# Kernel optimization log

Hardware: AMD Instinct MI355X
Metric: run time of the kernel (lower is better)

## Reference

```python
import jax, jax.numpy as jnp
import numpy as np
import math

HEADS = 6
EPS = 1e-6


def _ln(x, a, b):
    # torch custom LayerNorm: unbiased std, divide by (std + eps)
    m = x.mean(axis=-1, keepdims=True)
    s = jnp.std(x, axis=-1, keepdims=True, ddof=1)
    return a * (x - m) / (s + EPS) + b


def _msa(z, wq, bq, wk, bk, wv, bv, wo, bo):
    B, S, D = z.shape
    dk = D // HEADS
    def proj(w, bias):
        return (z @ w.T + bias).reshape(B, S, HEADS, dk).transpose(0, 2, 1, 3)
    q = proj(wq, bq)  # [B,h,S,dk]
    k = proj(wk, bk)
    v = proj(wv, bv)
    scores = jnp.einsum('bhqd,bhkd->bhqk', q, k) / math.sqrt(dk)  # [B,h,S,S]
    p = jax.nn.softmax(scores, axis=-1)
    o = jnp.einsum('bhqk,bhkd->bhqd', p, v)
    o = o.transpose(0, 2, 1, 3).reshape(B, S, D)
    return o @ wo.T + bo


def setup_inputs() -> dict:
    key = jax.random.key(0)
    ks = jax.random.split(key, 6)
    B, S, D = 2, 4096, 384
    sc = 0.02
    return {
        'x': jax.random.normal(ks[0], (B, S, D), dtype=jnp.float32),
        'a0': jnp.ones((D,), jnp.float32), 'b0': jnp.zeros((D,), jnp.float32),
        'ra0': jnp.ones((D,), jnp.float32), 'rb0': jnp.zeros((D,), jnp.float32),
        'ra1': jnp.ones((D,), jnp.float32), 'rb1': jnp.zeros((D,), jnp.float32),
        'wq': jax.random.normal(ks[1], (D, D), jnp.float32) * sc, 'bq': jnp.zeros((D,), jnp.float32),
        'wk': jax.random.normal(ks[2], (D, D), jnp.float32) * sc, 'bk': jnp.zeros((D,), jnp.float32),
        'wv': jax.random.normal(ks[3], (D, D), jnp.float32) * sc, 'bv': jnp.zeros((D,), jnp.float32),
        'wo': jax.random.normal(ks[4], (D, D), jnp.float32) * sc, 'bo': jnp.zeros((D,), jnp.float32),
    }


def reference(x, a0, b0, ra0, rb0, ra1, rb1, wq, bq, wk, bk, wv, bv, wo, bo):
    # Faithful to source: both residual connections invoke MSA (MLP is never
    # called in the original forward), and the input to MSA is LayerNorm'd
    # twice (residual_conn norm, then norm[0]). Dropout = 0 (eval).
    z = _ln(_ln(x, ra0, rb0), a0, b0)
    x = x + _msa(z, wq, bq, wk, bk, wv, bv, wo, bo)
    z = _ln(_ln(x, ra1, rb1), a0, b0)
    x = x + _msa(z, wq, bq, wk, bk, wv, bv, wo, bo)
    return x
```

## Files before the change

kernel.cpp:

```cpp
#include <hip/hip_runtime.h>
#include <hip/hip_bf16.h>
#include <math.h>

typedef __bf16 bf16;
typedef __bf16 bf16x2 __attribute__((ext_vector_type(2)));
typedef __bf16 bf16x4 __attribute__((ext_vector_type(4)));
typedef __bf16 bf16x8 __attribute__((ext_vector_type(8)));
typedef float  f32x2  __attribute__((ext_vector_type(2)));
typedef float  f32x4  __attribute__((ext_vector_type(4)));
typedef float  f32x16 __attribute__((ext_vector_type(16)));
typedef int    i32x2  __attribute__((ext_vector_type(2)));
typedef int    i32x4  __attribute__((ext_vector_type(4)));

#define SEQ 4096
#define DM  384
#define NH  6
#define DK  64
#define NB  2
#define NSPLIT 4
#define WN  (DM * DM)
#define EPSLN 1e-6f

__device__ __forceinline__ float ldT(const void* p, size_t i, int f32) {
    return f32 ? ((const float*)p)[i] : (float)(((const bf16*)p)[i]);
}

__global__ __launch_bounds__(256) void ln2_kernel(
    const void* __restrict__ x, int xf32,
    const float* __restrict__ ra, const float* __restrict__ rb,
    const float* __restrict__ a0, const float* __restrict__ b0, bf16* __restrict__ z)
{
    int row  = blockIdx.x * 4 + (threadIdx.x >> 6);
    int lane = threadIdx.x & 63;
    size_t base = (size_t)row * DM;

    float v[6];
    float s = 0.f;
    #pragma unroll
    for (int i = 0; i < 6; i++) { v[i] = ldT(x, base + lane + i * 64, xf32); s += v[i]; }
    #pragma unroll
    for (int off = 1; off < 64; off <<= 1) s += __shfl_xor(s, off);
    float m = s * (1.f / DM);
    float sq = 0.f;
    #pragma unroll
    for (int i = 0; i < 6; i++) { float d = v[i] - m; sq += d * d; }
    #pragma unroll
    for (int off = 1; off < 64; off <<= 1) sq += __shfl_xor(sq, off);
    float inv = 1.f / (sqrtf(sq * (1.f / (DM - 1))) + EPSLN);

    s = 0.f;
    #pragma unroll
    for (int i = 0; i < 6; i++) {
        int c = lane + i * 64;
        v[i] = ra[c] * (v[i] - m) * inv + rb[c];
        s += v[i];
    }
    #pragma unroll
    for (int off = 1; off < 64; off <<= 1) s += __shfl_xor(s, off);
    m = s * (1.f / DM);
    sq = 0.f;
    #pragma unroll
    for (int i = 0; i < 6; i++) { float d = v[i] - m; sq += d * d; }
    #pragma unroll
    for (int off = 1; off < 64; off <<= 1) sq += __shfl_xor(sq, off);
    inv = 1.f / (sqrtf(sq * (1.f / (DM - 1))) + EPSLN);

    bf16* zr = z + base;
    #pragma unroll
    for (int i = 0; i < 6; i++) {
        int c = lane + i * 64;
        zr[c] = (bf16)(a0[c] * (v[i] - m) * inv + b0[c]);
    }
}

__global__ __launch_bounds__(256) void qkv_kernel(
    const bf16* __restrict__ A,
    const float* __restrict__ wq, const float* __restrict__ wk, const float* __restrict__ wv,
    const float* __restrict__ bq, const float* __restrict__ bk, const float* __restrict__ bv,
    bf16* __restrict__ qkout, bf16* __restrict__ vt)
{
    const int z = blockIdx.z;
    const float* W    = (z == 0) ? wq : (z == 1) ? wk : wv;
    const float* bias = (z == 0) ? bq : (z == 1) ? bk : bv;

    const int t = threadIdx.x;
    const int wave = t >> 6, lane = t & 63;
    const int l15 = lane & 15, quad = lane >> 4;
    const int wr = wave >> 1, wc = wave & 1;
    const int m0 = blockIdx.x * 128;
    const int n0 = blockIdx.y * 64;

    __shared__ __attribute__((aligned(16))) bf16 As[128][72];
    __shared__ __attribute__((aligned(16))) bf16 Bs[64][72];

    const int r0 = t >> 2;
    const int c0 = (t & 3) * 16;

    const bf16*  aptr0 = A + (size_t)(m0 + r0) * DM + c0;
    const bf16*  aptr1 = A + (size_t)(m0 + 64 + r0) * DM + c0;
    const float* bptr  = W + (size_t)(n0 + r0) * DM + c0;

    bf16x8 ra00 = *(const bf16x8*)(aptr0);
    bf16x8 ra01 = *(const bf16x8*)(aptr0 + 8);
    bf16x8 ra10 = *(const bf16x8*)(aptr1);
    bf16x8 ra11 = *(const bf16x8*)(aptr1 + 8);
    f32x4 wv0 = *(const f32x4*)(bptr);
    f32x4 wv1 = *(const f32x4*)(bptr + 4);
    f32x4 wv2 = *(const f32x4*)(bptr + 8);
    f32x4 wv3 = *(const f32x4*)(bptr + 12);

    f32x4 acc[4][2];
    #pragma unroll
    for (int mi = 0; mi < 4; mi++)
        #pragma unroll
        for (int ni = 0; ni < 2; ni++) acc[mi][ni] = (f32x4){0.f, 0.f, 0.f, 0.f};

    for (int kk = 0; kk < DM; kk += 64) {
        __syncthreads();
        *(bf16x8*)&As[r0][c0]          = ra00;
        *(bf16x8*)&As[r0][c0 + 8]      = ra01;
        *(bf16x8*)&As[64 + r0][c0]     = ra10;
        *(bf16x8*)&As[64 + r0][c0 + 8] = ra11;
        {
            bf16x8 b0v, b1v;
            #pragma unroll
            for (int j = 0; j < 4; j++) {
                b0v[j] = (bf16)wv0[j]; b0v[4 + j] = (bf16)wv1[j];
                b1v[j] = (bf16)wv2[j]; b1v[4 + j] = (bf16)wv3[j];
            }
            *(bf16x8*)&Bs[r0][c0]     = b0v;
            *(bf16x8*)&Bs[r0][c0 + 8] = b1v;
        }
        __syncthreads();
        if (kk + 64 < DM) {
            ra00 = *(const bf16x8*)(aptr0 + kk + 64);
            ra01 = *(const bf16x8*)(aptr0 + kk + 64 + 8);
            ra10 = *(const bf16x8*)(aptr1 + kk + 64);
            ra11 = *(const bf16x8*)(aptr1 + kk + 64 + 8);
            wv0 = *(const f32x4*)(bptr + kk + 64);
            wv1 = *(const f32x4*)(bptr + kk + 64 + 4);
            wv2 = *(const f32x4*)(bptr + kk + 64 + 8);
            wv3 = *(const f32x4*)(bptr + kk + 64 + 12);
        }

        #pragma unroll
        for (int kc = 0; kc < 64; kc += 32) {
            bf16x8 af[4], bf[2];
            #pragma unroll
            for (int mi = 0; mi < 4; mi++)
                af[mi] = *(const bf16x8*)&As[wr * 64 + mi * 16 + l15][kc + quad * 8];
            #pragma unroll
            for (int ni = 0; ni < 2; ni++)
                bf[ni] = *(const bf16x8*)&Bs[wc * 32 + ni * 16 + l15][kc + quad * 8];
            #pragma unroll
            for (int mi = 0; mi < 4; mi++)
                #pragma unroll
                for (int ni = 0; ni < 2; ni++)
                    acc[mi][ni] = __builtin_amdgcn_mfma_f32_16x16x32_bf16(af[mi], bf[ni], acc[mi][ni], 0, 0, 0);
        }
    }

    if (z < 2) {
        bf16* out = qkout + (size_t)z * ((size_t)NB * SEQ * DM);
        #pragma unroll
        for (int ni = 0; ni < 2; ni++) {
            int col = n0 + wc * 32 + ni * 16 + l15;
            float bb = bias[col];
            #pragma unroll
            for (int mi = 0; mi < 4; mi++) {
                #pragma unroll
                for (int r = 0; r < 4; r++) {
                    int row = m0 + wr * 64 + mi * 16 + quad * 4 + r;
                    out[(size_t)row * DM + col] = (bf16)(acc[mi][ni][r] + bb);
                }
            }
        }
    } else {
        #pragma unroll
        for (int ni = 0; ni < 2; ni++) {
            int col = n0 + wc * 32 + ni * 16 + l15;
            int h = col >> 6, d = col & 63;
            float bb = bias[col];
            #pragma unroll
            for (int mi = 0; mi < 4; mi++) {
                int row0 = m0 + wr * 64 + mi * 16 + quad * 4;
                int b = row0 >> 12, s0 = row0 & (SEQ - 1);
                bf16x4 ov;
                #pragma unroll
                for (int r = 0; r < 4; r++) ov[r] = (bf16)(acc[mi][ni][r] + bb);
                *(bf16x4*)(vt + (((size_t)b * NH + h) * DK + d) * SEQ + s0) = ov;
            }
        }
    }
}

__device__ __forceinline__ bf16x8 combineA(
    const bf16* __restrict__ o0, const bf16* __restrict__ o1,
    const bf16* __restrict__ o2, const bf16* __restrict__ o3,
    const float* __restrict__ lsum, int row, int kcol)
{
    int b = row >> 12, s = row & (SEQ - 1);
    int h = kcol >> 6;
    const size_t S1 = (size_t)NB * NH * SEQ;
    size_t lidx = ((size_t)b * NH + h) * SEQ + s;
    float inv = 1.f / (lsum[lidx] + lsum[S1 + lidx] + lsum[2 * S1 + lidx] + lsum[3 * S1 + lidx]);
    size_t idx = (size_t)row * DM + kcol;
    bf16x8 a = *(const bf16x8*)(o0 + idx);
    bf16x8 c = *(const bf16x8*)(o1 + idx);
    bf16x8 d = *(const bf16x8*)(o2 + idx);
    bf16x8 e = *(const bf16x8*)(o3 + idx);
    bf16x8 r;
    #pragma unroll
    for (int j = 0; j < 8; j++)
        r[j] = (bf16)((((float)a[j] + (float)c[j]) + ((float)d[j] + (float)e[j])) * inv);
    return r;
}

__global__ __launch_bounds__(256) void proj_kernel(
    const bf16* __restrict__ o0, const bf16* __restrict__ o1,
    const bf16* __restrict__ o2, const bf16* __restrict__ o3,
    const float* __restrict__ lsum,
    const float* __restrict__ wo, const float* __restrict__ bo,
    const void* __restrict__ xin, int f32in,
    void* __restrict__ xout, int f32out)
{
    const int t = threadIdx.x;
    const int wave = t >> 6, lane = t & 63;
    const int l15 = lane & 15, quad = lane >> 4;
    const int wr = wave >> 1, wc = wave & 1;
    const int m0 = blockIdx.x * 64;
    const int n0 = blockIdx.y * 64;

    __shared__ __attribute__((aligned(16))) bf16 As[64][72];
    __shared__ __attribute__((aligned(16))) bf16 Bs[64][72];

    const int r0 = t >> 2;
    const int c0 = (t & 3) * 16;
    const int arow = m0 + r0;
    const float* bptr = wo + (size_t)(n0 + r0) * DM + c0;

    bf16x8 ca0 = combineA(o0, o1, o2, o3, lsum, arow, c0);
    bf16x8 ca1 = combineA(o0, o1, o2, o3, lsum, arow, c0 + 8);
    f32x4 wv0 = *(const f32x4*)(bptr);
    f32x4 wv1 = *(const f32x4*)(bptr + 4);
    f32x4 wv2 = *(const f32x4*)(bptr + 8);
    f32x4 wv3 = *(const f32x4*)(bptr + 12);

    f32x4 acc[2][2];
    #pragma unroll
    for (int mi = 0; mi < 2; mi++)
        #pragma unroll
        for (int ni = 0; ni < 2; ni++) acc[mi][ni] = (f32x4){0.f, 0.f, 0.f, 0.f};

    for (int kk = 0; kk < DM; kk += 64) {
        __syncthreads();
        *(bf16x8*)&As[r0][c0]     = ca0;
        *(bf16x8*)&As[r0][c0 + 8] = ca1;
        {
            bf16x8 b0v, b1v;
            #pragma unroll
            for (int j = 0; j < 4; j++) {
                b0v[j] = (bf16)wv0[j]; b0v[4 + j] = (bf16)wv1[j];
                b1v[j] = (bf16)wv2[j]; b1v[4 + j] = (bf16)wv3[j];
            }
            *(bf16x8*)&Bs[r0][c0]     = b0v;
            *(bf16x8*)&Bs[r0][c0 + 8] = b1v;
        }
        __syncthreads();
        if (kk + 64 < DM) {
            ca0 = combineA(o0, o1, o2, o3, lsum, arow, kk + 64 + c0);
            ca1 = combineA(o0, o1, o2, o3, lsum, arow, kk + 64 + c0 + 8);
            wv0 = *(const f32x4*)(bptr + kk + 64);
            wv1 = *(const f32x4*)(bptr + kk + 64 + 4);
            wv2 = *(const f32x4*)(bptr + kk + 64 + 8);
            wv3 = *(const f32x4*)(bptr + kk + 64 + 12);
        }

        #pragma unroll
        for (int kc = 0; kc < 64; kc += 32) {
            bf16x8 af[2], bf[2];
            #pragma unroll
            for (int mi = 0; mi < 2; mi++)
                af[mi] = *(const bf16x8*)&As[wr * 32 + mi * 16 + l15][kc + quad * 8];
            #pragma unroll
            for (int ni = 0; ni < 2; ni++)
                bf[ni] = *(const bf16x8*)&Bs[wc * 32 + ni * 16 + l15][kc + quad * 8];
            #pragma unroll
            for (int mi = 0; mi < 2; mi++)
                #pragma unroll
                for (int ni = 0; ni < 2; ni++)
                    acc[mi][ni] = __builtin_amdgcn_mfma_f32_16x16x32_bf16(af[mi], bf[ni], acc[mi][ni], 0, 0, 0);
        }
    }

    #pragma unroll
    for (int ni = 0; ni < 2; ni++) {
        int col = n0 + wc * 32 + ni * 16 + l15;
        float bb = bo[col];
        #pragma unroll
        for (int mi = 0; mi < 2; mi++) {
            #pragma unroll
            for (int r = 0; r < 4; r++) {
                size_t idx = (size_t)(m0 + wr * 32 + mi * 16 + quad * 4 + r) * DM + col;
                float val = ldT(xin, idx, f32in) + acc[mi][ni][r] + bb;
                if (f32out) ((float*)xout)[idx] = val;
                else        ((bf16*)xout)[idx] = (bf16)val;
            }
        }
    }
}

__device__ __forceinline__ unsigned packbf(float lo, float hi) {
    bf16x2 t;
    t[0] = (bf16)lo;
    t[1] = (bf16)hi;
    return __builtin_bit_cast(unsigned, t);
}

__device__ __forceinline__ i32x2 halfswap(unsigned a, unsigned b) {
#if defined(__has_builtin) && __has_builtin(__builtin_amdgcn_permlane32_swap)
    return __builtin_amdgcn_permlane32_swap((int)a, (int)b, false, false);
#else
    int pa = __shfl_xor((int)a, 32);
    int pb = __shfl_xor((int)b, 32);
    bool hi = (threadIdx.x & 32) != 0;
    i32x2 r;
    r[0] = hi ? pb : (int)a;
    r[1] = hi ? (int)b : pa;
    return r;
#endif
}

#define V_RS 40
#define V_TS 2576

__global__ __launch_bounds__(256, 4) void attn_kernel(
    const bf16* __restrict__ q, const bf16* __restrict__ k, const bf16* __restrict__ vt,
    bf16* __restrict__ o0, bf16* __restrict__ o1,
    bf16* __restrict__ o2, bf16* __restrict__ o3, float* __restrict__ lsum)
{
    int qt = blockIdx.x, h = blockIdx.y;
    int b = blockIdx.z >> 2, split = blockIdx.z & 3;
    const int t = threadIdx.x;
    const int wave = t >> 6, lane = t & 63;
    const int L = lane & 31, hf = lane >> 5;
    const int q0 = qt * 128;
    const int kvbase = split * (SEQ / NSPLIT);
    size_t basebh = (size_t)b * SEQ * DM + (size_t)h * DK;

    __shared__ __attribute__((aligned(16))) bf16 Ks[128][72];
    __shared__ __attribute__((aligned(16))) bf16 VtL[4 * V_TS];

    const float c2 = 0.18033688011112042f;
    const int qrow = q0 + wave * 32 + L;
    bf16x8 aq[4];
    {
        const bf16* qp = q + basebh + (size_t)qrow * DM + 8 * hf;
        #pragma unroll
        for (int ks = 0; ks < 4; ks++) {
            bf16x8 tq = *(const bf16x8*)(qp + 16 * ks);
            #pragma unroll
            for (int j = 0; j < 8; j++) tq[j] = (bf16)((float)tq[j] * c2);
            aq[ks] = tq;
        }
    }

    f32x2 lrv = (f32x2){0.f, 0.f};
    f32x16 oacc[2];
    #pragma unroll
    for (int db = 0; db < 2; db++)
        #pragma unroll
        for (int r = 0; r < 16; r++) oacc[db][r] = 0.f;

    f32x16 zf;
    #pragma unroll
    for (int r = 0; r < 16; r++) zf[r] = 0.f;

    const int sd  = t >> 2;
    const int sc  = t & 3;
    const bf16* vtrow0 = vt + (((size_t)b * NH + h) * DK + sd) * SEQ + sc * 32;
    const int skk = t >> 1;
    const int sdk = (t & 1) * 32;
    const bf16* krow0 = k + basebh + (size_t)skk * DM + sdk;

    bf16x8 vr0 = *(const bf16x8*)(vtrow0 + kvbase);
    bf16x8 vr1 = *(const bf16x8*)(vtrow0 + kvbase + 8);
    bf16x8 vr2 = *(const bf16x8*)(vtrow0 + kvbase + 16);
    bf16x8 vr3 = *(const bf16x8*)(vtrow0 + kvbase + 24);
    bf16x8 kr0 = *(const bf16x8*)(krow0 + (size_t)kvbase * DM);
    bf16x8 kr1 = *(const bf16x8*)(krow0 + (size_t)kvbase * DM + 8);
    bf16x8 kr2 = *(const bf16x8*)(krow0 + (size_t)kvbase * DM + 16);
    bf16x8 kr3 = *(const bf16x8*)(krow0 + (size_t)kvbase * DM + 24);

    for (int it = 0; it < SEQ / NSPLIT / 128; it++) {
        __syncthreads();
        {
            bf16* vw = &VtL[sc * V_TS + sd * V_RS];
            *(bf16x8*)(vw)      = vr0;
            *(bf16x8*)(vw + 8)  = vr1;
            *(bf16x8*)(vw + 16) = vr2;
            *(bf16x8*)(vw + 24) = vr3;
            *(bf16x8*)&Ks[skk][sdk]      = kr0;
            *(bf16x8*)&Ks[skk][sdk + 8]  = kr1;
            *(bf16x8*)&Ks[skk][sdk + 16] = kr2;
            *(bf16x8*)&Ks[skk][sdk + 24] = kr3;
        }
        __syncthreads();

        {
            int kvn = (it + 1 < SEQ / NSPLIT / 128) ? kvbase + (it + 1) * 128 : kvbase;
            const bf16* vp = vtrow0 + kvn;
            vr0 = *(const bf16x8*)(vp);
            vr1 = *(const bf16x8*)(vp + 8);
            vr2 = *(const bf16x8*)(vp + 16);
            vr3 = *(const bf16x8*)(vp + 24);
            const bf16* kp2 = krow0 + (size_t)kvn * DM;
            kr0 = *(const bf16x8*)(kp2);
            kr1 = *(const bf16x8*)(kp2 + 8);
            kr2 = *(const bf16x8*)(kp2 + 16);
            kr3 = *(const bf16x8*)(kp2 + 24);
        }

        #pragma unroll
        for (int kvb = 0; kvb < 4; kvb++) {
            f32x16 sacc;
            {
                bf16x8 kf = *(const bf16x8*)&Ks[kvb * 32 + L][hf * 8];
                sacc = __builtin_amdgcn_mfma_f32_32x32x16_bf16(kf, aq[0], zf, 0, 0, 0);
            }
            #pragma unroll
            for (int ks = 1; ks < 4; ks++) {
                bf16x8 kf = *(const bf16x8*)&Ks[kvb * 32 + L][ks * 16 + hf * 8];
                sacc = __builtin_amdgcn_mfma_f32_32x32x16_bf16(kf, aq[ks], sacc, 0, 0, 0);
            }

            float p[16];
            #pragma unroll
            for (int r = 0; r < 16; r++) p[r] = __builtin_amdgcn_exp2f(sacc[r]);
            #pragma unroll
            for (int r = 0; r < 16; r += 2)
                lrv += (f32x2){p[r], p[r + 1]};

            unsigned pk0[4], pk1[4];
            #pragma unroll
            for (int R = 0; R < 4; R++) {
                pk0[R] = packbf(p[4 * R], p[4 * R + 1]);
                pk1[R] = packbf(p[4 * R + 2], p[4 * R + 3]);
            }

            #pragma unroll
            for (int ci = 0; ci < 2; ci++) {
                i32x2 r0 = halfswap(pk0[2 * ci], pk0[2 * ci + 1]);
                i32x2 r1 = halfswap(pk1[2 * ci], pk1[2 * ci + 1]);
                i32x4 w;
                w[0] = r0[0]; w[1] = r1[0]; w[2] = r0[1]; w[3] = r1[1];
                bf16x8 pb = __builtin_bit_cast(bf16x8, w);
                #pragma unroll
                for (int db = 0; db < 2; db++) {
                    bf16x8 av = *(const bf16x8*)&VtL[kvb * V_TS + (db * 32 + L) * V_RS
                                                     + ci * 16 + hf * 8];
                    oacc[db] = __builtin_amdgcn_mfma_f32_32x32x16_bf16(av, pb, oacc[db], 0, 0, 0);
                }
            }
        }
    }

    bf16* osel = (split == 0) ? o0 : (split == 1) ? o1 : (split == 2) ? o2 : o3;
    float lrow = lrv[0] + lrv[1];
    lrow += __shfl_xor(lrow, 32);
    bf16* op = osel + basebh + (size_t)qrow * DM;
    #pragma unroll
    for (int db = 0; db < 2; db++) {
        #pragma unroll
        for (int R = 0; R < 4; R++) {
            bf16x4 ov;
            #pragma unroll
            for (int r = 0; r < 4; r++) ov[r] = (bf16)oacc[db][4 * R + r];
            *(bf16x4*)(op + db * 32 + R * 8 + hf * 4) = ov;
        }
    }
    if (hf == 0)
        lsum[(size_t)split * (NB * NH * SEQ) + ((size_t)b * NH + h) * SEQ + qrow] = lrow;
}

extern "C" void kernel_launch(void* const* d_in, const int* in_sizes, int n_in,
                              void* d_out, int out_size, void* d_ws, size_t ws_size,
                              hipStream_t stream) {
    const size_t SZ = (size_t)NB * SEQ * DM;

    const float* x   = (const float*)d_in[0];
    const float* a0  = (const float*)d_in[1];
    const float* b0  = (const float*)d_in[2];
    const float* ra0 = (const float*)d_in[3];
    const float* rb0 = (const float*)d_in[4];
    const float* ra1 = (const float*)d_in[5];
    const float* rb1 = (const float*)d_in[6];
    const float* wq  = (const float*)d_in[7];  const float* bq = (const float*)d_in[8];
    const float* wk  = (const float*)d_in[9];  const float* bk = (const float*)d_in[10];
    const float* wv  = (const float*)d_in[11]; const float* bv = (const float*)d_in[12];
    const float* wo  = (const float*)d_in[13]; const float* bo = (const float*)d_in[14];

    bf16* zob = (bf16*)d_ws;
    bf16* qb  = zob + SZ;
    bf16* kb  = qb + SZ;
    bf16* vtb = kb + SZ;
    bf16* x1  = vtb + SZ;
    bf16* o1b = x1 + SZ;
    bf16* o2b = o1b + SZ;
    bf16* o3b = o2b + SZ;
    float* lsum = (float*)(o3b + SZ);

    dim3 gLN(NB * SEQ / 4);
    dim3 gG(NB * SEQ / 128, DM / 64, 3);
    dim3 gP(NB * SEQ / 64, DM / 64);
    dim3 gA(SEQ / 128, NH, NB * NSPLIT);

    ln2_kernel<<<gLN, 256, 0, stream>>>(x, 1, ra0, rb0, a0, b0, zob);
    qkv_kernel<<<gG, 256, 0, stream>>>(zob, wq, wk, wv, bq, bk, bv, qb, vtb);
    attn_kernel<<<gA, 256, 0, stream>>>(qb, kb, vtb, zob, o1b, o2b, o3b, lsum);
    proj_kernel<<<gP, 256, 0, stream>>>(zob, o1b, o2b, o3b, lsum, wo, bo, x, 1, x1, 0);
    ln2_kernel<<<gLN, 256, 0, stream>>>(x1, 0, ra1, rb1, a0, b0, zob);
    qkv_kernel<<<gG, 256, 0, stream>>>(zob, wq, wk, wv, bq, bk, bv, qb, vtb);
    attn_kernel<<<gA, 256, 0, stream>>>(qb, kb, vtb, zob, o1b, o2b, o3b, lsum);
    proj_kernel<<<gP, 256, 0, stream>>>(zob, o1b, o2b, o3b, lsum, wo, bo, x1, 0, d_out, 1);
}
```

Before: 309.2 us.

## Stage K/V tiles via direct global-to-LDS loads with double buffering and swizzle

Result: no change. 308.3 us (-0.3%).

```diff
diff --git a/kernel.cpp b/kernel.cpp
--- a/kernel.cpp
+++ b/kernel.cpp
@@ -331,10 +331,16 @@
 #endif
 }
 
-#define V_RS 40
-#define V_TS 2576
-
-__global__ __launch_bounds__(256, 4) void attn_kernel(
+typedef __attribute__((address_space(3))) unsigned int        lds_u32;
+typedef __attribute__((address_space(1))) const unsigned int  glb_u32;
+
+__device__ __forceinline__ void gload16(const void* g, void* l) {
+    __builtin_amdgcn_global_load_lds((glb_u32*)g, (lds_u32*)l, 16, 0, 0);
+}
+
+#define KV_IT (SEQ / NSPLIT / 128)
+
+__global__ __launch_bounds__(256, 2) void attn_kernel(
     const bf16* __restrict__ q, const bf16* __restrict__ k, const bf16* __restrict__ vt,
     bf16* __restrict__ o0, bf16* __restrict__ o1,
     bf16* __restrict__ o2, bf16* __restrict__ o3, float* __restrict__ lsum)
@@ -348,8 +354,8 @@
     const int kvbase = split * (SEQ / NSPLIT);
     size_t basebh = (size_t)b * SEQ * DM + (size_t)h * DK;
 
-    __shared__ __attribute__((aligned(16))) bf16 Ks[128][72];
-    __shared__ __attribute__((aligned(16))) bf16 VtL[4 * V_TS];
+    __shared__ __attribute__((aligned(16))) unsigned char Kb[2][128 * 64 * 2];
+    __shared__ __attribute__((aligned(16))) unsigned char Vb[2][64 * 128 * 2];
 
     const float c2 = 0.18033688011112042f;
     const int qrow = q0 + wave * 32 + L;
@@ -376,61 +382,55 @@
     #pragma unroll
     for (int r = 0; r < 16; r++) zf[r] = 0.f;
 
-    const int sd  = t >> 2;
-    const int sc  = t & 3;
-    const bf16* vtrow0 = vt + (((size_t)b * NH + h) * DK + sd) * SEQ + sc * 32;
-    const int skk = t >> 1;
-    const int sdk = (t & 1) * 32;
-    const bf16* krow0 = k + basebh + (size_t)skk * DM + sdk;
-
-    bf16x8 vr0 = *(const bf16x8*)(vtrow0 + kvbase);
-    bf16x8 vr1 = *(const bf16x8*)(vtrow0 + kvbase + 8);
-    bf16x8 vr2 = *(const bf16x8*)(vtrow0 + kvbase + 16);
-    bf16x8 vr3 = *(const bf16x8*)(vtrow0 + kvbase + 24);
-    bf16x8 kr0 = *(const bf16x8*)(krow0 + (size_t)kvbase * DM);
-    bf16x8 kr1 = *(const bf16x8*)(krow0 + (size_t)kvbase * DM + 8);
-    bf16x8 kr2 = *(const bf16x8*)(krow0 + (size_t)kvbase * DM + 16);
-    bf16x8 kr3 = *(const bf16x8*)(krow0 + (size_t)kvbase * DM + 24);
-
-    for (int it = 0; it < SEQ / NSPLIT / 128; it++) {
-        __syncthreads();
-        {
-            bf16* vw = &VtL[sc * V_TS + sd * V_RS];
-            *(bf16x8*)(vw)      = vr0;
-            *(bf16x8*)(vw + 8)  = vr1;
-            *(bf16x8*)(vw + 16) = vr2;
-            *(bf16x8*)(vw + 24) = vr3;
-            *(bf16x8*)&Ks[skk][sdk]      = kr0;
-            *(bf16x8*)&Ks[skk][sdk + 8]  = kr1;
-            *(bf16x8*)&Ks[skk][sdk + 16] = kr2;
-            *(bf16x8*)&Ks[skk][sdk + 24] = kr3;
-        }
-        __syncthreads();
-
-        {
-            int kvn = (it + 1 < SEQ / NSPLIT / 128) ? kvbase + (it + 1) * 128 : kvbase;
-            const bf16* vp = vtrow0 + kvn;
-            vr0 = *(const bf16x8*)(vp);
-            vr1 = *(const bf16x8*)(vp + 8);
-            vr2 = *(const bf16x8*)(vp + 16);
-            vr3 = *(const bf16x8*)(vp + 24);
-            const bf16* kp2 = krow0 + (size_t)kvn * DM;
-            kr0 = *(const bf16x8*)(kp2);
-            kr1 = *(const bf16x8*)(kp2 + 8);
-            kr2 = *(const bf16x8*)(kp2 + 16);
-            kr3 = *(const bf16x8*)(kp2 + 24);
-        }
+    const bf16* kg0 = k + basebh + (size_t)(kvbase + wave * 64 + (lane >> 3)) * DM
+                        + ((lane & 7) ^ (lane >> 3)) * 8;
+    const int vd = (wave - 2) * 32 + (lane >> 4);
+    const bf16* vg0 = vt + (((size_t)b * NH + h) * DK + vd) * SEQ + kvbase;
+    const int kvE = ((lane & 15) ^ (lane >> 4)) * 8;
+    const int kvO = ((lane & 15) ^ 4 ^ (lane >> 4)) * 8;
+
+    auto STAGE = [&](int bufi, int kvoff) {
+        if (wave < 2) {
+            const bf16* g = kg0 + (size_t)kvoff * DM;
+            unsigned char* lb = &Kb[bufi][wave * 8192];
+            #pragma unroll
+            for (int c = 0; c < 8; c++)
+                gload16(g + (size_t)c * 8 * DM, lb + c * 1024);
+        } else {
+            const bf16* g = vg0 + kvoff;
+            unsigned char* lb = &Vb[bufi][(wave - 2) * 8192];
+            #pragma unroll
+            for (int c = 0; c < 8; c++)
+                gload16(g + (size_t)c * 4 * SEQ + ((c & 1) ? kvO : kvE), lb + c * 1024);
+        }
+    };
+
+    STAGE(0, 0);
+    STAGE(1, 128);
+
+    const int sw = (L & 7) << 4;
+    int koff[4];
+    #pragma unroll
+    for (int ks = 0; ks < 4; ks++) koff[ks] = (ks * 32 + hf * 16) ^ sw;
+
+    for (int it = 0; it < KV_IT; it++) {
+        const int bufi = it & 1;
+        asm volatile("s_waitcnt vmcnt(8)" ::: "memory");
+        __builtin_amdgcn_s_barrier();
+
+        const unsigned char* KbP = Kb[bufi];
+        const unsigned char* VbP = Vb[bufi];
 
         #pragma unroll
         for (int kvb = 0; kvb < 4; kvb++) {
             f32x16 sacc;
             {
-                bf16x8 kf = *(const bf16x8*)&Ks[kvb * 32 + L][hf * 8];
+                bf16x8 kf = *(const bf16x8*)(KbP + (kvb * 32 + L) * 128 + koff[0]);
                 sacc = __builtin_amdgcn_mfma_f32_32x32x16_bf16(kf, aq[0], zf, 0, 0, 0);
             }
             #pragma unroll
             for (int ks = 1; ks < 4; ks++) {
-                bf16x8 kf = *(const bf16x8*)&Ks[kvb * 32 + L][ks * 16 + hf * 8];
+                bf16x8 kf = *(const bf16x8*)(KbP + (kvb * 32 + L) * 128 + koff[ks]);
                 sacc = __builtin_amdgcn_mfma_f32_32x32x16_bf16(kf, aq[ks], sacc, 0, 0, 0);
             }
 
@@ -457,13 +457,21 @@
                 bf16x8 pb = __builtin_bit_cast(bf16x8, w);
                 #pragma unroll
                 for (int db = 0; db < 2; db++) {
-                    bf16x8 av = *(const bf16x8*)&VtL[kvb * V_TS + (db * 32 + L) * V_RS
-                                                     + ci * 16 + hf * 8];
+                    bf16x8 av = *(const bf16x8*)(VbP + (db * 32 + L) * 256
+                                  + ((kvb * 64 + ci * 32 + hf * 16) ^ sw));
                     oacc[db] = __builtin_amdgcn_mfma_f32_32x32x16_bf16(av, pb, oacc[db], 0, 0, 0);
                 }
             }
         }
-    }
+
+        asm volatile("s_waitcnt lgkmcnt(0)" ::: "memory");
+        __builtin_amdgcn_s_barrier();
+
+        int kv2 = (it + 2 < KV_IT) ? (it + 2) * 128 : 0;
+        STAGE(bufi, kv2);
+    }
+
+    asm volatile("s_waitcnt vmcnt(0)" ::: "memory");
 
     bf16* osel = (split == 0) ? o0 : (split == 1) ? o1 : (split == 2) ? o2 : o3;
     float lrow = lrv[0] + lrv[1];
```

## Load V operands directly from global memory instead of staging through LDS

Applied to the files above, without the earlier changes.

Result: slower. 426.2 us (+37.8%).

```diff
diff --git a/kernel.cpp b/kernel.cpp
--- a/kernel.cpp
+++ b/kernel.cpp
@@ -331,8 +331,7 @@
 #endif
 }
 
-#define V_RS 40
-#define V_TS 2576
+#define KV_IT (SEQ / NSPLIT / 128)
 
 __global__ __launch_bounds__(256, 4) void attn_kernel(
     const bf16* __restrict__ q, const bf16* __restrict__ k, const bf16* __restrict__ vt,
@@ -349,7 +348,6 @@
     size_t basebh = (size_t)b * SEQ * DM + (size_t)h * DK;
 
     __shared__ __attribute__((aligned(16))) bf16 Ks[128][72];
-    __shared__ __attribute__((aligned(16))) bf16 VtL[4 * V_TS];
 
     const float c2 = 0.18033688011112042f;
     const int qrow = q0 + wave * 32 + L;
@@ -376,54 +374,41 @@
     #pragma unroll
     for (int r = 0; r < 16; r++) zf[r] = 0.f;
 
-    const int sd  = t >> 2;
-    const int sc  = t & 3;
-    const bf16* vtrow0 = vt + (((size_t)b * NH + h) * DK + sd) * SEQ + sc * 32;
+    const bf16* vrow0 = vt + (((size_t)b * NH + h) * DK + L) * SEQ + kvbase + hf * 8;
+    const bf16* vrow1 = vrow0 + (size_t)32 * SEQ;
+
     const int skk = t >> 1;
     const int sdk = (t & 1) * 32;
     const bf16* krow0 = k + basebh + (size_t)skk * DM + sdk;
 
-    bf16x8 vr0 = *(const bf16x8*)(vtrow0 + kvbase);
-    bf16x8 vr1 = *(const bf16x8*)(vtrow0 + kvbase + 8);
-    bf16x8 vr2 = *(const bf16x8*)(vtrow0 + kvbase + 16);
-    bf16x8 vr3 = *(const bf16x8*)(vtrow0 + kvbase + 24);
     bf16x8 kr0 = *(const bf16x8*)(krow0 + (size_t)kvbase * DM);
     bf16x8 kr1 = *(const bf16x8*)(krow0 + (size_t)kvbase * DM + 8);
     bf16x8 kr2 = *(const bf16x8*)(krow0 + (size_t)kvbase * DM + 16);
     bf16x8 kr3 = *(const bf16x8*)(krow0 + (size_t)kvbase * DM + 24);
 
-    for (int it = 0; it < SEQ / NSPLIT / 128; it++) {
+    for (int it = 0; it < KV_IT; it++) {
         __syncthreads();
-        {
-            bf16* vw = &VtL[sc * V_TS + sd * V_RS];
-            *(bf16x8*)(vw)      = vr0;
-            *(bf16x8*)(vw + 8)  = vr1;
-            *(bf16x8*)(vw + 16) = vr2;
-            *(bf16x8*)(vw + 24) = vr3;
-            *(bf16x8*)&Ks[skk][sdk]      = kr0;
-            *(bf16x8*)&Ks[skk][sdk + 8]  = kr1;
-            *(bf16x8*)&Ks[skk][sdk + 16] = kr2;
-            *(bf16x8*)&Ks[skk][sdk + 24] = kr3;
-        }
+        *(bf16x8*)&Ks[skk][sdk]      = kr0;
+        *(bf16x8*)&Ks[skk][sdk + 8]  = kr1;
+        *(bf16x8*)&Ks[skk][sdk + 16] = kr2;
+        *(bf16x8*)&Ks[skk][sdk + 24] = kr3;
         __syncthreads();
 
-        {
-            int kvn = (it + 1 < SEQ / NSPLIT / 128) ? kvbase + (it + 1) * 128 : kvbase;
-            const bf16* vp = vtrow0 + kvn;
-            vr0 = *(const bf16x8*)(vp);
-            vr1 = *(const bf16x8*)(vp + 8);
-            vr2 = *(const bf16x8*)(vp + 16);
-            vr3 = *(const bf16x8*)(vp + 24);
-            const bf16* kp2 = krow0 + (size_t)kvn * DM;
+        if (it + 1 < KV_IT) {
+            const bf16* kp2 = krow0 + (size_t)(kvbase + (it + 1) * 128) * DM;
             kr0 = *(const bf16x8*)(kp2);
             kr1 = *(const bf16x8*)(kp2 + 8);
             kr2 = *(const bf16x8*)(kp2 + 16);
             kr3 = *(const bf16x8*)(kp2 + 24);
         }
 
+        const bf16* v0 = vrow0 + it * 128;
+        const bf16* v1 = vrow1 + it * 128;
+
         #pragma unroll
         for (int kvb = 0; kvb < 4; kvb++) {
             f32x16 sacc;
+            __builtin_amdgcn_s_setprio(1);
             {
                 bf16x8 kf = *(const bf16x8*)&Ks[kvb * 32 + L][hf * 8];
                 sacc = __builtin_amdgcn_mfma_f32_32x32x16_bf16(kf, aq[0], zf, 0, 0, 0);
@@ -433,6 +418,7 @@
                 bf16x8 kf = *(const bf16x8*)&Ks[kvb * 32 + L][ks * 16 + hf * 8];
                 sacc = __builtin_amdgcn_mfma_f32_32x32x16_bf16(kf, aq[ks], sacc, 0, 0, 0);
             }
+            __builtin_amdgcn_s_setprio(0);
 
             float p[16];
             #pragma unroll
@@ -448,6 +434,7 @@
                 pk1[R] = packbf(p[4 * R + 2], p[4 * R + 3]);
             }
 
+            __builtin_amdgcn_s_setprio(1);
             #pragma unroll
             for (int ci = 0; ci < 2; ci++) {
                 i32x2 r0 = halfswap(pk0[2 * ci], pk0[2 * ci + 1]);
@@ -455,13 +442,12 @@
                 i32x4 w;
                 w[0] = r0[0]; w[1] = r1[0]; w[2] = r0[1]; w[3] = r1[1];
                 bf16x8 pb = __builtin_bit_cast(bf16x8, w);
-                #pragma unroll
-                for (int db = 0; db < 2; db++) {
-                    bf16x8 av = *(const bf16x8*)&VtL[kvb * V_TS + (db * 32 + L) * V_RS
-                                                     + ci * 16 + hf * 8];
-                    oacc[db] = __builtin_amdgcn_mfma_f32_32x32x16_bf16(av, pb, oacc[db], 0, 0, 0);
-                }
-            }
+                bf16x8 av0 = *(const bf16x8*)(v0 + kvb * 32 + ci * 16);
+                bf16x8 av1 = *(const bf16x8*)(v1 + kvb * 32 + ci * 16);
+                oacc[0] = __builtin_amdgcn_mfma_f32_32x32x16_bf16(av0, pb, oacc[0], 0, 0, 0);
+                oacc[1] = __builtin_amdgcn_mfma_f32_32x32x16_bf16(av1, pb, oacc[1], 0, 0, 0);
+            }
+            __builtin_amdgcn_s_setprio(0);
         }
     }
 
```
